# Kernel tuning notes

Hardware: AMD Instinct MI355X
Metric: run time of the kernel (lower is better)

The kernel has to match this reference:

```python
import jax, jax.numpy as jnp
import numpy as np

DIM = 1024
HEADS = 16
DIM_HEAD = 64
SCALE = DIM_HEAD ** -0.5


def setup_inputs() -> dict:
    key = jax.random.key(0)
    k1, k2, k3, k4 = jax.random.split(key, 4)
    B, N = 2, 2048
    x = jax.random.normal(k1, (B, N, DIM), dtype=jnp.float32)
    mask = jnp.ones((B, N), dtype=bool)
    gamma = jnp.ones((DIM,), dtype=jnp.float32)
    # init like nn.Linear default ~ U(-1/sqrt(fan_in), 1/sqrt(fan_in)); gaussian * 0.02 is fine numerically
    Wq = jax.random.normal(k2, (DIM, HEADS * DIM_HEAD), dtype=jnp.float32) * 0.02
    Wkv = jax.random.normal(k3, (DIM, HEADS * DIM_HEAD * 2), dtype=jnp.float32) * 0.02
    Wo = jax.random.normal(k4, (HEADS * DIM_HEAD, DIM), dtype=jnp.float32) * 0.02
    return {"x": x, "mask": mask, "gamma": gamma, "Wq": Wq, "Wkv": Wkv, "Wo": Wo}


def _rmsnorm(x, gamma):
    # F.normalize(x, dim=-1) * sqrt(dim) * gamma ; eps clamp matches torch (1e-12)
    n = jnp.sqrt(jnp.sum(x * x, axis=-1, keepdims=True))
    return x / jnp.maximum(n, 1e-12) * (DIM ** 0.5) * gamma


def reference(x, mask, gamma, Wq, Wkv, Wo):
    B, N, _ = x.shape
    xn = _rmsnorm(x, gamma)
    q = xn @ Wq                      # [b, n, h*d]
    kv = xn @ Wkv                    # [b, n, 2*h*d] (self-attention: context = x)
    k, v = jnp.split(kv, 2, axis=-1)

    def to_heads(t):
        return t.reshape(B, N, HEADS, DIM_HEAD).transpose(0, 2, 1, 3)  # b h n d

    q, k, v = to_heads(q), to_heads(k), to_heads(v)

    sim = jnp.einsum('bhid,bhjd->bhij', q, k) * SCALE
    neg = -jnp.finfo(sim.dtype).max
    # key padding mask: b j -> b 1 1 j
    sim = jnp.where(mask[:, None, None, :], sim, neg)
    # causal: triu(j - i + 1) with i == j -> strict upper triangle masked
    causal_mask = jnp.triu(jnp.ones((N, N), dtype=bool), k=1)
    sim = jnp.where(causal_mask, neg, sim)

    attn = jax.nn.softmax(sim, axis=-1)
    out = jnp.einsum('bhij,bhjd->bhid', attn, v)
    out = out.transpose(0, 2, 1, 3).reshape(B, N, HEADS * DIM_HEAD)
    return out @ Wo
```

## Files before the change

kernel.cpp:

```cpp
#include <hip/hip_runtime.h>
#include <hip/hip_bf16.h>
#include <stdint.h>

#define NSEQ 2048
#define NB 2
#define NTOK (NB*NSEQ)

typedef __attribute__((ext_vector_type(8))) short bf16x8;
typedef __attribute__((ext_vector_type(4))) float f32x4;

#if __has_builtin(__builtin_amdgcn_exp2f)
#define EXP2F(x) __builtin_amdgcn_exp2f(x)
#else
#define EXP2F(x) __expf((x) * 0.69314718056f)
#endif

__device__ __forceinline__ unsigned short f2bf(float f) {
  __hip_bfloat16 h = __float2bfloat16(f);
  return *reinterpret_cast<unsigned short*>(&h);
}

__device__ __forceinline__ unsigned cvt_pk_bf16(float a, float b) {
  unsigned r;
  asm("v_cvt_pk_bf16_f32 %0, %1, %2" : "=v"(r) : "v"(a), "v"(b));
  return r;
}

__device__ __forceinline__ void gload_lds16(const void* g, void* l) {
  __builtin_amdgcn_global_load_lds(
      (const __attribute__((address_space(1))) void*)(uintptr_t)g,
      (__attribute__((address_space(3))) void*)(uintptr_t)l,
      16, 0, 0);
}

__global__ __launch_bounds__(256) void rmsnorm_cast(
    const float* __restrict__ x, const float* __restrict__ gamma,
    unsigned short* __restrict__ xn)
{
  const int row = blockIdx.x;
  const float4 v = ((const float4*)(x + (size_t)row*1024))[threadIdx.x];
  float ss = v.x*v.x + v.y*v.y + v.z*v.z + v.w*v.w;
  #pragma unroll
  for (int o = 32; o >= 1; o >>= 1) ss += __shfl_xor(ss, o);
  __shared__ float wsum[4];
  if ((threadIdx.x & 63) == 0) wsum[threadIdx.x >> 6] = ss;
  __syncthreads();
  const float tot = wsum[0] + wsum[1] + wsum[2] + wsum[3];
  const float f = 32.0f / fmaxf(sqrtf(tot), 1e-12f);
  const float4 g = ((const float4*)gamma)[threadIdx.x];
  ushort4 o;
  o.x = f2bf(v.x * f * g.x);
  o.y = f2bf(v.y * f * g.y);
  o.z = f2bf(v.z * f * g.z);
  o.w = f2bf(v.w * f * g.w);
  ((ushort4*)(xn + (size_t)row*1024))[threadIdx.x] = o;
}

__global__ __launch_bounds__(256) void transpose_cast_all(
    const float* __restrict__ Wq, const float* __restrict__ Wkv,
    const float* __restrict__ Wo, unsigned short* __restrict__ WallT,
    unsigned short* __restrict__ WoT, float qscale)
{
  const int bx = blockIdx.x;
  const float* src; unsigned short* dst; int C; float scale; int cblk;
  if (bx < 16)      { src = Wq;  dst = WallT;               C = 1024; scale = qscale; cblk = bx; }
  else if (bx < 48) { src = Wkv; dst = WallT + 1024*1024;   C = 2048; scale = 1.0f;   cblk = bx - 16; }
  else              { src = Wo;  dst = WoT;                 C = 1024; scale = 1.0f;   cblk = bx - 48; }

  __shared__ float t[64][65];
  const int lx = threadIdx.x & 63, ly = threadIdx.x >> 6;
  const int c0 = cblk * 64, r0 = blockIdx.y * 64;
  #pragma unroll
  for (int i = 0; i < 16; ++i) {
    const int r = ly + i*4;
    t[r][lx] = src[(size_t)(r0 + r)*C + c0 + lx];
  }
  __syncthreads();
  #pragma unroll
  for (int i = 0; i < 16; ++i) {
    const int r = ly + i*4;
    dst[(size_t)(c0 + r)*1024 + r0 + lx] = f2bf(t[lx][r] * scale);
  }
}

template<int MODE>
__global__ __launch_bounds__(256) void gemm_bt(
    const unsigned short* __restrict__ A, const unsigned short* __restrict__ BT,
    void* __restrict__ Cp, unsigned short* __restrict__ Vt, int M, int N, int K)
{
  __shared__ __align__(16) unsigned short As[3][128*32];
  __shared__ __align__(16) unsigned short Bs[3][128*32];
  const int tid = threadIdx.x, lane = tid & 63, wv = tid >> 6;
  const int wm = wv >> 1, wn = wv & 1;
  const int m0 = blockIdx.y * 128, n0 = blockIdx.x * 128;
  const int g = lane >> 4, l15 = lane & 15;

  f32x4 acc[4][4];
  #pragma unroll
  for (int i = 0; i < 4; ++i)
    #pragma unroll
    for (int j = 0; j < 4; ++j) acc[i][j] = f32x4{0.f,0.f,0.f,0.f};

  auto STAGE = [&](int buf, int kt) {
    const int k0 = kt * 32;
    #pragma unroll
    for (int j = 0; j < 2; ++j) {
      const int c = wv*128 + j*64 + lane;
      const int row = c >> 2;
      const int kc = (c & 3) ^ ((row >> 1) & 3);
      gload_lds16(A  + (size_t)(m0 + row)*K + k0 + kc*8, As[buf] + (size_t)(wv*128 + j*64)*8);
      gload_lds16(BT + (size_t)(n0 + row)*K + k0 + kc*8, Bs[buf] + (size_t)(wv*128 + j*64)*8);
    }
  };

  const int nk = K >> 5;
  STAGE(0, 0);
  STAGE(1, 1);
  int cur = 0, sb = 2;
  for (int kt = 0; kt < nk; ++kt) {
    if (kt + 1 < nk) { asm volatile("s_waitcnt vmcnt(4)" ::: "memory"); }
    else             { asm volatile("s_waitcnt vmcnt(0)" ::: "memory"); }
    __builtin_amdgcn_s_barrier();
    __builtin_amdgcn_sched_barrier(0);

    bf16x8 af[4], bfr[4];
    #pragma unroll
    for (int mt = 0; mt < 4; ++mt) {
      const int row = wm*64 + mt*16 + l15;
      af[mt] = *(const bf16x8*)(As[cur] + row*32 + ((g ^ ((row >> 1) & 3)) << 3));
    }
    #pragma unroll
    for (int nt = 0; nt < 4; ++nt) {
      const int col = wn*64 + nt*16 + l15;
      bfr[nt] = *(const bf16x8*)(Bs[cur] + col*32 + ((g ^ ((col >> 1) & 3)) << 3));
    }
    if (kt + 2 < nk) STAGE(sb, kt + 2);
    #pragma unroll
    for (int mt = 0; mt < 4; ++mt)
      #pragma unroll
      for (int nt = 0; nt < 4; ++nt)
        acc[mt][nt] = __builtin_amdgcn_mfma_f32_16x16x32_bf16(af[mt], bfr[nt], acc[mt][nt], 0, 0, 0);

    cur = (cur == 2) ? 0 : cur + 1;
    sb  = (sb  == 2) ? 0 : sb  + 1;
  }

  if (MODE == 2 && n0 >= 2048) {
    #pragma unroll
    for (int mt = 0; mt < 4; ++mt)
      #pragma unroll
      for (int nt = 0; nt < 4; ++nt) {
        const int row = m0 + wm*64 + mt*16 + g*4;
        const int col = n0 + wn*64 + nt*16 + l15;
        const f32x4 v = acc[mt][nt];
        ushort4 o;
        o.x = f2bf(v[0]); o.y = f2bf(v[1]); o.z = f2bf(v[2]); o.w = f2bf(v[3]);
        *(ushort4*)(Vt + ((size_t)((row >> 11)*1024 + (col - 2048)))*2048 + (row & 2047)) = o;
      }
    return;
  }

  #pragma unroll
  for (int mt = 0; mt < 4; ++mt)
    #pragma unroll
    for (int nt = 0; nt < 4; ++nt) {
      const int row = m0 + wm*64 + mt*16 + g*4;
      const int col = n0 + wn*64 + nt*16 + l15;
      const f32x4 v = acc[mt][nt];
      #pragma unroll
      for (int r = 0; r < 4; ++r) {
        if (MODE != 0) ((unsigned short*)Cp)[(size_t)(row + r)*N + col] = f2bf(v[r]);
        else           ((float*)Cp)[(size_t)(row + r)*N + col] = v[r];
      }
    }
}

__global__ __launch_bounds__(512, 4) void attn_fwd(
    const unsigned short* __restrict__ QKV,
    const unsigned short* __restrict__ Vt,
    unsigned short* __restrict__ AO)
{
  __shared__ __align__(16) unsigned char smem[81920];

  const int bh = blockIdx.x, k = blockIdx.y;
  const int qlo = k, qhi = 31 - k;
  const int b = bh >> 4, h = bh & 15;
  const int tid = threadIdx.x, lane = tid & 63, wv = tid >> 6;
  const int quad = wv >> 2, w4 = wv & 3;
  const int g = lane >> 4, q15 = lane & 15;
  const int qrow_lo = qlo*64 + w4*16 + q15;
  const int qrow_hi = qhi*64 + w4*16 + q15;

  unsigned short* Kb = (unsigned short*)(smem + quad*32768);
  unsigned short* Vb = (unsigned short*)(smem + quad*32768 + 16384);
  unsigned short* Plw = (unsigned short*)(smem + 65536 + wv*2048);

  const unsigned short* Qlo = QKV + (size_t)(b*NSEQ + qrow_lo)*3072 + h*64;
  const unsigned short* Qhi = QKV + (size_t)(b*NSEQ + qrow_hi)*3072 + h*64;
  const bf16x8 qlo0 = *(const bf16x8*)(Qlo + g*8);
  const bf16x8 qlo1 = *(const bf16x8*)(Qlo + 32 + g*8);
  const bf16x8 qhi0 = *(const bf16x8*)(Qhi + g*8);
  const bf16x8 qhi1 = *(const bf16x8*)(Qhi + 32 + g*8);

  const bf16x8 ones = { (short)0x3F80, (short)0x3F80, (short)0x3F80, (short)0x3F80,
                        (short)0x3F80, (short)0x3F80, (short)0x3F80, (short)0x3F80 };

  f32x4 l_lo = f32x4{0.f,0.f,0.f,0.f}, l_hi = f32x4{0.f,0.f,0.f,0.f};
  f32x4 olo[4], ohi[4];
  #pragma unroll
  for (int i = 0; i < 4; ++i) { olo[i] = f32x4{0.f,0.f,0.f,0.f}; ohi[i] = f32x4{0.f,0.f,0.f,0.f}; }

  auto STAGE = [&](int buf, int kt) {
    const int kv0 = kt * 64;
    #pragma unroll
    for (int j = 0; j < 2; ++j) {
      const int c = w4*128 + j*64 + lane;
      const int row = c >> 3;
      const int kc = (c & 7) ^ (row & 7);
      gload_lds16(QKV + (size_t)(b*NSEQ + kv0 + row)*3072 + 1024 + h*64 + kc*8,
                  Kb + (size_t)buf*4096 + (size_t)(w4*128 + j*64)*8);
      gload_lds16(Vt + (size_t)(bh*64 + row)*NSEQ + kv0 + kc*8,
                  Vb + (size_t)buf*4096 + (size_t)(w4*128 + j*64)*8);
    }
  };

  auto COMPUTE = [&](const bf16x8& qf0, const bf16x8& qf1, int qrow,
                     f32x4& lacc, f32x4* oacc, bool diag, int cur, int kv0) {
    f32x4 s[4];
    const unsigned short* Kc = Kb + (size_t)cur*4096;
    __builtin_amdgcn_s_setprio(1);
    #pragma unroll
    for (int st = 0; st < 4; ++st) {
      f32x4 a = f32x4{0.f,0.f,0.f,0.f};
      const int row = st*16 + q15;
      const int sw = row & 7;
      const bf16x8 kf0 = *(const bf16x8*)(Kc + row*64 + ((g ^ sw) << 3));
      const bf16x8 kf1 = *(const bf16x8*)(Kc + row*64 + (((4 | g) ^ sw) << 3));
      a = __builtin_amdgcn_mfma_f32_16x16x32_bf16(kf0, qf0, a, 0, 0, 0);
      a = __builtin_amdgcn_mfma_f32_16x16x32_bf16(kf1, qf1, a, 0, 0, 0);
      s[st] = a;
    }
    __builtin_amdgcn_s_setprio(0);

    if (diag) {
      #pragma unroll
      for (int st = 0; st < 4; ++st)
        #pragma unroll
        for (int r = 0; r < 4; ++r) {
          const int kvg = kv0 + st*16 + g*4 + r;
          if (kvg > qrow) s[st][r] = -1e30f;
        }
    }

    #pragma unroll
    for (int st = 0; st < 4; ++st) {
      const float p0 = EXP2F(s[st][0] - 12.0f);
      const float p1 = EXP2F(s[st][1] - 12.0f);
      const float p2 = EXP2F(s[st][2] - 12.0f);
      const float p3 = EXP2F(s[st][3] - 12.0f);
      const int base = (q15 << 6) + ((((st << 1) | (g >> 1)) ^ (q15 & 7)) << 3) + ((g & 1) << 2);
      uint2 w;
      w.x = cvt_pk_bf16(p0, p1);
      w.y = cvt_pk_bf16(p2, p3);
      *(uint2*)(Plw + base) = w;
    }

    const unsigned short* Vc = Vb + (size_t)cur*4096;
    __builtin_amdgcn_s_setprio(1);
    #pragma unroll
    for (int ks = 0; ks < 2; ++ks) {
      const bf16x8 pf = *(const bf16x8*)(Plw + (q15 << 6) + ((((ks << 2) | g) ^ (q15 & 7)) << 3));
      lacc = __builtin_amdgcn_mfma_f32_16x16x32_bf16(pf, ones, lacc, 0, 0, 0);
      #pragma unroll
      for (int dt = 0; dt < 4; ++dt) {
        const int dr = dt*16 + q15;
        const bf16x8 vf = *(const bf16x8*)(Vc + dr*64 + ((((ks << 2) | g) ^ (dr & 7)) << 3));
        oacc[dt] = __builtin_amdgcn_mfma_f32_16x16x32_bf16(pf, vf, oacc[dt], 0, 0, 0);
      }
    }
    __builtin_amdgcn_s_setprio(0);
  };

  STAGE(0, quad);
  __syncthreads();
  int cur = 0;
  for (int i = 0; i < 16; ++i) {
    const int t = quad + 2*i;
    const int tn = t + 2;
    if (tn <= qhi) STAGE(cur ^ 1, tn);
    if (t <= qhi) COMPUTE(qhi0, qhi1, qrow_hi, l_hi, ohi, t == qhi, cur, t*64);
    if (t <= qlo) COMPUTE(qlo0, qlo1, qrow_lo, l_lo, olo, t == qlo, cur, t*64);
    __syncthreads();
    cur ^= 1;
  }

  float* OHI = (float*)smem;
  float* OLO = (float*)(smem + 16384);
  float* LH  = (float*)(smem + 32768);
  float* LL  = (float*)(smem + 33024);

  if (quad == 1) {
    #pragma unroll
    for (int dt = 0; dt < 4; ++dt) {
      *(f32x4*)(OHI + ((w4*64 + lane)*4 + dt)*4) = ohi[dt];
      *(f32x4*)(OLO + ((w4*64 + lane)*4 + dt)*4) = olo[dt];
    }
    if (q15 == 0) {
      #pragma unroll
      for (int r = 0; r < 4; ++r) {
        LH[w4*16 + g*4 + r] = l_hi[r];
        LL[w4*16 + g*4 + r] = l_lo[r];
      }
    }
  }
  __syncthreads();
  if (quad == 0) {
    f32x4 ph[4], pl[4];
    #pragma unroll
    for (int dt = 0; dt < 4; ++dt) {
      ph[dt] = *(const f32x4*)(OHI + ((w4*64 + lane)*4 + dt)*4);
      pl[dt] = *(const f32x4*)(OLO + ((w4*64 + lane)*4 + dt)*4);
    }
    #pragma unroll
    for (int r = 0; r < 4; ++r) {
      const int row = g*4 + r;
      {
        const float inv = 1.0f / (l_hi[r] + LH[w4*16 + row]);
        const int qr = qhi*64 + w4*16 + row;
        #pragma unroll
        for (int dt = 0; dt < 4; ++dt)
          AO[(size_t)(b*NSEQ + qr)*1024 + h*64 + dt*16 + q15] =
              f2bf((ohi[dt][r] + ph[dt][r]) * inv);
      }
      {
        const float inv = 1.0f / (l_lo[r] + LL[w4*16 + row]);
        const int qr = qlo*64 + w4*16 + row;
        #pragma unroll
        for (int dt = 0; dt < 4; ++dt)
          AO[(size_t)(b*NSEQ + qr)*1024 + h*64 + dt*16 + q15] =
              f2bf((olo[dt][r] + pl[dt][r]) * inv);
      }
    }
  }
}

extern "C" void kernel_launch(void* const* d_in, const int* in_sizes, int n_in,
                              void* d_out, int out_size, void* d_ws, size_t ws_size,
                              hipStream_t stream) {
  (void)in_sizes; (void)n_in; (void)out_size; (void)ws_size;
  const float* x     = (const float*)d_in[0];
  const float* gamma = (const float*)d_in[2];
  const float* Wq    = (const float*)d_in[3];
  const float* Wkv   = (const float*)d_in[4];
  const float* Wo    = (const float*)d_in[5];
  float* out = (float*)d_out;

  char* ws = (char*)d_ws;
  unsigned short* xn    = (unsigned short*)(ws);
  unsigned short* AO    = xn;
  unsigned short* WallT = (unsigned short*)(ws + (size_t)(8u  << 20));
  unsigned short* WoT   = (unsigned short*)(ws + (size_t)(14u << 20));
  unsigned short* QKV   = (unsigned short*)(ws + (size_t)(16u << 20));
  unsigned short* Vt    = (unsigned short*)(ws + (size_t)(40u << 20));

  const float QSCALE = 0.125f * 1.44269504f;

  rmsnorm_cast<<<NTOK, 256, 0, stream>>>(x, gamma, xn);
  transpose_cast_all<<<dim3(64, 16), 256, 0, stream>>>(Wq, Wkv, Wo, WallT, WoT, QSCALE);
  gemm_bt<2><<<dim3(3072/128, 4096/128), 256, 0, stream>>>(xn, WallT, (void*)QKV, Vt, 4096, 3072, 1024);
  attn_fwd<<<dim3(32, 16), 512, 0, stream>>>(QKV, Vt, AO);
  gemm_bt<0><<<dim3(1024/128, 4096/128), 256, 0, stream>>>(AO, WoT, (void*)out, nullptr, 4096, 1024, 1024);
}
```

Before: 95.61 us.

## Fuse rmsnorm and weight transpose kernels; use 8-wave GEMM blocks

Merges the rmsnorm-cast and weight transpose-cast kernels into one launch, with block index ranges selecting the work, which removes one kernel launch and lets both run concurrently. The GEMM now uses 512-thread blocks of 8 waves arranged 2x4, each computing a 64x32 subtile with half the accumulators. The load staging and waitcnt are adjusted to the thread count. This aims to increase wave occupancy and latency hiding, at the cost of more LDS reads per MFMA, since A fragments are re-read by more waves.

```diff
diff --git a/kernel.cpp b/kernel.cpp
--- a/kernel.cpp
+++ b/kernel.cpp
@@ -33,43 +33,42 @@
       16, 0, 0);
 }
 
-__global__ __launch_bounds__(256) void rmsnorm_cast(
+__global__ __launch_bounds__(256) void prep_fused(
     const float* __restrict__ x, const float* __restrict__ gamma,
-    unsigned short* __restrict__ xn)
-{
-  const int row = blockIdx.x;
-  const float4 v = ((const float4*)(x + (size_t)row*1024))[threadIdx.x];
-  float ss = v.x*v.x + v.y*v.y + v.z*v.z + v.w*v.w;
-  #pragma unroll
-  for (int o = 32; o >= 1; o >>= 1) ss += __shfl_xor(ss, o);
-  __shared__ float wsum[4];
-  if ((threadIdx.x & 63) == 0) wsum[threadIdx.x >> 6] = ss;
-  __syncthreads();
-  const float tot = wsum[0] + wsum[1] + wsum[2] + wsum[3];
-  const float f = 32.0f / fmaxf(sqrtf(tot), 1e-12f);
-  const float4 g = ((const float4*)gamma)[threadIdx.x];
-  ushort4 o;
-  o.x = f2bf(v.x * f * g.x);
-  o.y = f2bf(v.y * f * g.y);
-  o.z = f2bf(v.z * f * g.z);
-  o.w = f2bf(v.w * f * g.w);
-  ((ushort4*)(xn + (size_t)row*1024))[threadIdx.x] = o;
-}
-
-__global__ __launch_bounds__(256) void transpose_cast_all(
+    unsigned short* __restrict__ xn,
     const float* __restrict__ Wq, const float* __restrict__ Wkv,
     const float* __restrict__ Wo, unsigned short* __restrict__ WallT,
     unsigned short* __restrict__ WoT, float qscale)
 {
-  const int bx = blockIdx.x;
+  __shared__ float t[64][65];
+  const int bid = blockIdx.x;
+  if (bid < NTOK) {
+    const int row = bid;
+    const float4 v = ((const float4*)(x + (size_t)row*1024))[threadIdx.x];
+    float ss = v.x*v.x + v.y*v.y + v.z*v.z + v.w*v.w;
+    #pragma unroll
+    for (int o = 32; o >= 1; o >>= 1) ss += __shfl_xor(ss, o);
+    if ((threadIdx.x & 63) == 0) t[0][threadIdx.x >> 6] = ss;
+    __syncthreads();
+    const float tot = t[0][0] + t[0][1] + t[0][2] + t[0][3];
+    const float f = 32.0f / fmaxf(sqrtf(tot), 1e-12f);
+    const float4 g = ((const float4*)gamma)[threadIdx.x];
+    ushort4 o;
+    o.x = f2bf(v.x * f * g.x);
+    o.y = f2bf(v.y * f * g.y);
+    o.z = f2bf(v.z * f * g.z);
+    o.w = f2bf(v.w * f * g.w);
+    ((ushort4*)(xn + (size_t)row*1024))[threadIdx.x] = o;
+    return;
+  }
+  const int tb = bid - NTOK;
+  const int bx = tb & 63, by = tb >> 6;
   const float* src; unsigned short* dst; int C; float scale; int cblk;
   if (bx < 16)      { src = Wq;  dst = WallT;               C = 1024; scale = qscale; cblk = bx; }
   else if (bx < 48) { src = Wkv; dst = WallT + 1024*1024;   C = 2048; scale = 1.0f;   cblk = bx - 16; }
   else              { src = Wo;  dst = WoT;                 C = 1024; scale = 1.0f;   cblk = bx - 48; }
-
-  __shared__ float t[64][65];
   const int lx = threadIdx.x & 63, ly = threadIdx.x >> 6;
-  const int c0 = cblk * 64, r0 = blockIdx.y * 64;
+  const int c0 = cblk * 64, r0 = by * 64;
   #pragma unroll
   for (int i = 0; i < 16; ++i) {
     const int r = ly + i*4;
@@ -84,33 +83,30 @@
 }
 
 template<int MODE>
-__global__ __launch_bounds__(256) void gemm_bt(
+__global__ __launch_bounds__(512, 6) void gemm_w8(
     const unsigned short* __restrict__ A, const unsigned short* __restrict__ BT,
     void* __restrict__ Cp, unsigned short* __restrict__ Vt, int M, int N, int K)
 {
   __shared__ __align__(16) unsigned short As[3][128*32];
   __shared__ __align__(16) unsigned short Bs[3][128*32];
   const int tid = threadIdx.x, lane = tid & 63, wv = tid >> 6;
-  const int wm = wv >> 1, wn = wv & 1;
+  const int wm = wv >> 2, wn = wv & 3;
   const int m0 = blockIdx.y * 128, n0 = blockIdx.x * 128;
   const int g = lane >> 4, l15 = lane & 15;
 
-  f32x4 acc[4][4];
+  f32x4 acc[4][2];
   #pragma unroll
   for (int i = 0; i < 4; ++i)
     #pragma unroll
-    for (int j = 0; j < 4; ++j) acc[i][j] = f32x4{0.f,0.f,0.f,0.f};
+    for (int j = 0; j < 2; ++j) acc[i][j] = f32x4{0.f,0.f,0.f,0.f};
 
   auto STAGE = [&](int buf, int kt) {
     const int k0 = kt * 32;
-    #pragma unroll
-    for (int j = 0; j < 2; ++j) {
-      const int c = wv*128 + j*64 + lane;
-      const int row = c >> 2;
-      const int kc = (c & 3) ^ ((row >> 1) & 3);
-      gload_lds16(A  + (size_t)(m0 + row)*K + k0 + kc*8, As[buf] + (size_t)(wv*128 + j*64)*8);
-      gload_lds16(BT + (size_t)(n0 + row)*K + k0 + kc*8, Bs[buf] + (size_t)(wv*128 + j*64)*8);
-    }
+    const int c = wv*64 + lane;
+    const int row = c >> 2;
+    const int kc = (c & 3) ^ ((row >> 1) & 3);
+    gload_lds16(A  + (size_t)(m0 + row)*K + k0 + kc*8, As[buf] + (size_t)c*8);
+    gload_lds16(BT + (size_t)(n0 + row)*K + k0 + kc*8, Bs[buf] + (size_t)c*8);
   };
 
   const int nk = K >> 5;
@@ -118,27 +114,27 @@
   STAGE(1, 1);
   int cur = 0, sb = 2;
   for (int kt = 0; kt < nk; ++kt) {
-    if (kt + 1 < nk) { asm volatile("s_waitcnt vmcnt(4)" ::: "memory"); }
+    if (kt + 1 < nk) { asm volatile("s_waitcnt vmcnt(2)" ::: "memory"); }
     else             { asm volatile("s_waitcnt vmcnt(0)" ::: "memory"); }
     __builtin_amdgcn_s_barrier();
     __builtin_amdgcn_sched_barrier(0);
 
-    bf16x8 af[4], bfr[4];
+    bf16x8 af[4], bfr[2];
     #pragma unroll
     for (int mt = 0; mt < 4; ++mt) {
       const int row = wm*64 + mt*16 + l15;
       af[mt] = *(const bf16x8*)(As[cur] + row*32 + ((g ^ ((row >> 1) & 3)) << 3));
     }
     #pragma unroll
-    for (int nt = 0; nt < 4; ++nt) {
-      const int col = wn*64 + nt*16 + l15;
+    for (int nt = 0; nt < 2; ++nt) {
+      const int col = wn*32 + nt*16 + l15;
       bfr[nt] = *(const bf16x8*)(Bs[cur] + col*32 + ((g ^ ((col >> 1) & 3)) << 3));
     }
     if (kt + 2 < nk) STAGE(sb, kt + 2);
     #pragma unroll
     for (int mt = 0; mt < 4; ++mt)
       #pragma unroll
-      for (int nt = 0; nt < 4; ++nt)
+      for (int nt = 0; nt < 2; ++nt)
         acc[mt][nt] = __builtin_amdgcn_mfma_f32_16x16x32_bf16(af[mt], bfr[nt], acc[mt][nt], 0, 0, 0);
 
     cur = (cur == 2) ? 0 : cur + 1;
@@ -149,9 +145,9 @@
     #pragma unroll
     for (int mt = 0; mt < 4; ++mt)
       #pragma unroll
-      for (int nt = 0; nt < 4; ++nt) {
+      for (int nt = 0; nt < 2; ++nt) {
         const int row = m0 + wm*64 + mt*16 + g*4;
-        const int col = n0 + wn*64 + nt*16 + l15;
+        const int col = n0 + wn*32 + nt*16 + l15;
         const f32x4 v = acc[mt][nt];
         ushort4 o;
         o.x = f2bf(v[0]); o.y = f2bf(v[1]); o.z = f2bf(v[2]); o.w = f2bf(v[3]);
@@ -163,9 +159,9 @@
   #pragma unroll
   for (int mt = 0; mt < 4; ++mt)
     #pragma unroll
-    for (int nt = 0; nt < 4; ++nt) {
+    for (int nt = 0; nt < 2; ++nt) {
       const int row = m0 + wm*64 + mt*16 + g*4;
-      const int col = n0 + wn*64 + nt*16 + l15;
+      const int col = n0 + wn*32 + nt*16 + l15;
       const f32x4 v = acc[mt][nt];
       #pragma unroll
       for (int r = 0; r < 4; ++r) {
@@ -365,9 +361,8 @@
 
   const float QSCALE = 0.125f * 1.44269504f;
 
-  rmsnorm_cast<<<NTOK, 256, 0, stream>>>(x, gamma, xn);
-  transpose_cast_all<<<dim3(64, 16), 256, 0, stream>>>(Wq, Wkv, Wo, WallT, WoT, QSCALE);
-  gemm_bt<2><<<dim3(3072/128, 4096/128), 256, 0, stream>>>(xn, WallT, (void*)QKV, Vt, 4096, 3072, 1024);
+  prep_fused<<<NTOK + 1024, 256, 0, stream>>>(x, gamma, xn, Wq, Wkv, Wo, WallT, WoT, QSCALE);
+  gemm_w8<2><<<dim3(3072/128, 4096/128), 512, 0, stream>>>(xn, WallT, (void*)QKV, Vt, 4096, 3072, 1024);
   attn_fwd<<<dim3(32, 16), 512, 0, stream>>>(QKV, Vt, AO);
-  gemm_bt<0><<<dim3(1024/128, 4096/128), 256, 0, stream>>>(AO, WoT, (void*)out, nullptr, 4096, 1024, 1024);
-}
+  gemm_w8<0><<<dim3(1024/128, 4096/128), 512, 0, stream>>>(AO, WoT, (void*)out, nullptr, 4096, 1024, 1024);
+}
```

Result: faster. 92.73 us (-3.0%).
